# Optimization experiments

Hardware: AMD Instinct MI355X
Metric: run time of the kernel (lower is better)

## Reference

```python
import jax, jax.numpy as jnp
import numpy as np

DIM = 1152
NUM_HEADS = 16
HEAD_DIM = DIM // NUM_HEADS
EPS = 1e-6
B, N, M = 4, 4096, 512


def setup_inputs() -> dict:
    key = jax.random.key(0)
    ks = jax.random.split(key, 12)
    s = 0.02
    return {
        "x": jax.random.normal(ks[0], (B, N, DIM), dtype=jnp.float32),
        "cond": jax.random.normal(ks[1], (B, M, DIM), dtype=jnp.float32),
        "kv_seqlen": jax.random.randint(ks[2], (B,), 1, M + 1, dtype=jnp.int32),
        "q_w": jax.random.normal(ks[3], (DIM, DIM), dtype=jnp.float32) * s,
        "q_b": jnp.zeros((DIM,), jnp.float32),
        "kv_w": jax.random.normal(ks[4], (DIM, 2 * DIM), dtype=jnp.float32) * s,
        "kv_b": jnp.zeros((2 * DIM,), jnp.float32),
        "proj_w": jax.random.normal(ks[5], (DIM, DIM), dtype=jnp.float32) * s,
        "proj_b": jnp.zeros((DIM,), jnp.float32),
        "qn_w": jnp.ones((HEAD_DIM,), jnp.float32),
        "kn_w": jnp.ones((HEAD_DIM,), jnp.float32),
    }


def _rmsnorm_fp32(t, w):
    # RMSNorm computed in fp32 over head_dim, then cast back
    t32 = t.astype(jnp.float32)
    inv = jax.lax.rsqrt(jnp.mean(t32 * t32, axis=-1, keepdims=True) + EPS)
    return ((t32 * inv) * w.astype(jnp.float32)).astype(t.dtype)


def reference(x, cond, kv_seqlen, q_w, q_b, kv_w, kv_b, proj_w, proj_b, qn_w, kn_w):
    b, n, c = x.shape
    out_dtype = x.dtype
    q = (x @ q_w + q_b).reshape(b, n, NUM_HEADS, HEAD_DIM)           # [B,N,H,D]
    kv = (cond @ kv_w + kv_b).reshape(b, -1, 2, NUM_HEADS, HEAD_DIM)
    k, v = kv[:, :, 0], kv[:, :, 1]                                   # [B,M,H,D]
    q = _rmsnorm_fp32(q, qn_w)
    k = _rmsnorm_fp32(k, kn_w)
    # original casts to bf16 for the attention kernel when out_dtype is fp32
    q16, k16, v16 = q.astype(jnp.bfloat16), k.astype(jnp.bfloat16), v.astype(jnp.bfloat16)
    scale = 1.0 / np.sqrt(HEAD_DIM)
    scores = jnp.einsum("bnhd,bmhd->bhnm", q16, k16,
                        preferred_element_type=jnp.float32) * scale   # [B,H,N,M] fp32
    m = cond.shape[1]
    valid = (jnp.arange(m)[None, :] < kv_seqlen[:, None])             # [B,M] ragged kv mask
    scores = jnp.where(valid[:, None, None, :], scores, -jnp.inf)
    probs = jax.nn.softmax(scores, axis=-1).astype(jnp.bfloat16)
    out = jnp.einsum("bhnm,bmhd->bnhd", probs, v16).reshape(b, n, c)
    out = out.astype(out_dtype)
    return out @ proj_w + proj_b
```

## Files before the change

kernel.cpp:

```cpp
#include <hip/hip_runtime.h>
#include <math.h>

typedef unsigned short ushort_t;
typedef __attribute__((ext_vector_type(4))) float floatx4;
typedef __attribute__((ext_vector_type(8))) short bf16x8;

#define DIMC 1152
#define NHEADS 16
#define HDIM 72

__device__ __forceinline__ ushort_t f2bf(float f) {
  unsigned u = __float_as_uint(f);
  u += 0x7FFFu + ((u >> 16) & 1u);
  return (ushort_t)(u >> 16);
}
__device__ __forceinline__ float bf2f(ushort_t s) {
  return __uint_as_float(((unsigned)s) << 16);
}

__device__ __forceinline__ void gload_lds16(const ushort_t* g, ushort_t* l) {
  __builtin_amdgcn_global_load_lds(
      (const __attribute__((address_space(1))) unsigned int*)(const void*)g,
      (__attribute__((address_space(3))) unsigned int*)(void*)l, 16, 0, 0);
}

__device__ __forceinline__ bf16x8 load_bf16x8(const ushort_t* p) {
  union { bf16x8 v; uint4 u; } t;
  t.u = *(const uint4*)p;
  return t.v;
}

__global__ void cvt_bf16_kernel(const float* __restrict__ src,
                                ushort_t* __restrict__ dst, int n8) {
  int i = blockIdx.x * 256 + threadIdx.x;
  if (i >= n8) return;
  float4 f0 = ((const float4*)src)[2 * (size_t)i];
  float4 f1 = ((const float4*)src)[2 * (size_t)i + 1];
  union { ushort_t s[8]; uint4 u; } t;
  t.s[0] = f2bf(f0.x); t.s[1] = f2bf(f0.y); t.s[2] = f2bf(f0.z); t.s[3] = f2bf(f0.w);
  t.s[4] = f2bf(f1.x); t.s[5] = f2bf(f1.y); t.s[6] = f2bf(f1.z); t.s[7] = f2bf(f1.w);
  ((uint4*)dst)[i] = t.u;
}

__global__ void transpose_w_kernel(const float* __restrict__ W,
                                   ushort_t* __restrict__ Wt, int K, int N) {
  __shared__ ushort_t tile[64 * 80];
  int k0 = blockIdx.x * 64, n0 = blockIdx.y * 64;
  int tid = threadIdx.x;
  int kl = tid >> 4, n4 = tid & 15;
  for (int rr = 0; rr < 4; rr++) {
    int k = kl + rr * 16;
    float4 f = *(const float4*)(W + (size_t)(k0 + k) * N + n0 + n4 * 4);
    tile[(n4 * 4 + 0) * 80 + k] = f2bf(f.x);
    tile[(n4 * 4 + 1) * 80 + k] = f2bf(f.y);
    tile[(n4 * 4 + 2) * 80 + k] = f2bf(f.z);
    tile[(n4 * 4 + 3) * 80 + k] = f2bf(f.w);
  }
  __syncthreads();
  int nl = tid >> 2, kq = tid & 3;
  uint4 v0 = *(const uint4*)(tile + nl * 80 + kq * 16);
  uint4 v1 = *(const uint4*)(tile + nl * 80 + kq * 16 + 8);
  *(uint4*)(Wt + (size_t)(n0 + nl) * K + k0 + kq * 16) = v0;
  *(uint4*)(Wt + (size_t)(n0 + nl) * K + k0 + kq * 16 + 8) = v1;
}

template <bool OUT_F32>
__global__ __launch_bounds__(256, 3) void gemm128_kernel(
    const ushort_t* __restrict__ A0, const ushort_t* __restrict__ Bt0,
    const float* __restrict__ bias0, void* __restrict__ C0,
    int NTn0, int Ncols0,
    const ushort_t* __restrict__ A1, const ushort_t* __restrict__ Bt1,
    const float* __restrict__ bias1, void* __restrict__ C1,
    int NTn1, int Ncols1,
    int nblk0, int Kdim) {
  __shared__ ushort_t S[24576];

  int lin = blockIdx.x;
  int cpx = gridDim.x >> 3;
  int wg = (lin & 7) * cpx + (lin >> 3);

  const ushort_t* Aseg; const ushort_t* Bseg;
  const float* bias; void* Cptr; int NTn, Ncols;
  if (wg < nblk0) {
    Aseg = A0; Bseg = Bt0; bias = bias0; Cptr = C0; NTn = NTn0; Ncols = Ncols0;
  } else {
    wg -= nblk0;
    Aseg = A1; Bseg = Bt1; bias = bias1; Cptr = C1; NTn = NTn1; Ncols = Ncols1;
  }
  int mt = wg / NTn, nt = wg % NTn;
  int m0 = mt * 128, n0 = nt * 128;

  int tid = threadIdx.x;
  int wid = tid >> 6, lane = tid & 63, quad = lane >> 4, l16 = lane & 15;
  int wr = wid >> 1, wc = wid & 1;
  const int qoff = (quad * 8) ^ ((l16 & 8) << 1);

  const int srow = tid >> 2;
  const int scol = ((tid & 3) * 8) ^ ((tid & 32) ? 16 : 0);
  const ushort_t* Abase = Aseg + (size_t)m0 * Kdim;
  const ushort_t* Bbase = Bseg + (size_t)n0 * Kdim;

  auto stageA = [&](int t, int buf) {
    const ushort_t* src = Abase + (size_t)srow * Kdim + t * 32 + scol;
    ushort_t* dst = S + buf * 8192 + (tid >> 6) * 512;
    gload_lds16(src, dst);
    gload_lds16(src + (size_t)64 * Kdim, dst + 2048);
  };
  auto stageB = [&](int t, int buf) {
    const ushort_t* src = Bbase + (size_t)srow * Kdim + t * 32 + scol;
    ushort_t* dst = S + buf * 8192 + 4096 + (tid >> 6) * 512;
    gload_lds16(src, dst);
    gload_lds16(src + (size_t)64 * Kdim, dst + 2048);
  };

  floatx4 zero = {0.f, 0.f, 0.f, 0.f};
  floatx4 acc[4][4];
#pragma unroll
  for (int i = 0; i < 4; i++)
#pragma unroll
    for (int j = 0; j < 4; j++) acc[i][j] = zero;

  int NT = Kdim >> 5;

  stageA(0, 0); stageB(0, 0);
  stageA(1, 1); stageB(1, 1);
  asm volatile("s_waitcnt vmcnt(4)" ::: "memory");
  __builtin_amdgcn_s_barrier();

  int cur = 0;
  for (int t = 0; t < NT; ++t) {
    int nx2 = cur + 2; if (nx2 >= 3) nx2 -= 3;
    const int base = cur * 8192;
    const int arow = base + (wr * 64 + l16) * 32 + qoff;
    const int brow = base + 4096 + (wc * 64 + l16) * 32 + qoff;

    bf16x8 bfr[4], a01[2];
#pragma unroll
    for (int c = 0; c < 4; c++)
      bfr[c] = *(const bf16x8*)(S + brow + c * 512);
    a01[0] = *(const bf16x8*)(S + arow);
    a01[1] = *(const bf16x8*)(S + arow + 512);
    if (t + 2 < NT) stageA(t + 2, nx2);
    __builtin_amdgcn_s_barrier();
    asm volatile("s_waitcnt lgkmcnt(0)" ::: "memory");
    __builtin_amdgcn_sched_barrier(0);
    __builtin_amdgcn_s_setprio(1);
#pragma unroll
    for (int c = 0; c < 4; c++) {
      acc[0][c] = __builtin_amdgcn_mfma_f32_16x16x32_bf16(a01[0], bfr[c], acc[0][c], 0, 0, 0);
      acc[1][c] = __builtin_amdgcn_mfma_f32_16x16x32_bf16(a01[1], bfr[c], acc[1][c], 0, 0, 0);
    }
    __builtin_amdgcn_s_setprio(0);
    __builtin_amdgcn_s_barrier();

    bf16x8 a23[2];
    a23[0] = *(const bf16x8*)(S + arow + 1024);
    a23[1] = *(const bf16x8*)(S + arow + 1536);
    if (t + 2 < NT) stageB(t + 2, nx2);
    __builtin_amdgcn_s_barrier();
    asm volatile("s_waitcnt lgkmcnt(0)" ::: "memory");
    __builtin_amdgcn_sched_barrier(0);
    __builtin_amdgcn_s_setprio(1);
#pragma unroll
    for (int c = 0; c < 4; c++) {
      acc[2][c] = __builtin_amdgcn_mfma_f32_16x16x32_bf16(a23[0], bfr[c], acc[2][c], 0, 0, 0);
      acc[3][c] = __builtin_amdgcn_mfma_f32_16x16x32_bf16(a23[1], bfr[c], acc[3][c], 0, 0, 0);
    }
    __builtin_amdgcn_s_setprio(0);
    if (t + 2 < NT)
      asm volatile("s_waitcnt vmcnt(4)" ::: "memory");
    else
      asm volatile("s_waitcnt vmcnt(0)" ::: "memory");
    __builtin_amdgcn_s_barrier();

    cur = cur + 1; if (cur == 3) cur = 0;
  }

  float bv[4];
#pragma unroll
  for (int c = 0; c < 4; c++) bv[c] = bias[n0 + wc * 64 + c * 16 + l16];
#pragma unroll
  for (int mf = 0; mf < 4; mf++)
#pragma unroll
    for (int c = 0; c < 4; c++)
#pragma unroll
      for (int r = 0; r < 4; r++) {
        int row = m0 + wr * 64 + mf * 16 + quad * 4 + r;
        int col = n0 + wc * 64 + c * 16 + l16;
        float v = acc[mf][c][r] + bv[c];
        if constexpr (OUT_F32)
          ((float*)Cptr)[(size_t)row * Ncols + col] = v;
        else
          ((ushort_t*)Cptr)[(size_t)row * Ncols + col] = f2bf(v);
      }
}

__global__ void rmsnorm_heads_kernel(ushort_t* __restrict__ p,
                                     const float* __restrict__ w,
                                     int rowstride) {
  int gw = blockIdx.x * 4 + (threadIdx.x >> 6);
  int lane = threadIdx.x & 63;
  int row = gw >> 4, h = gw & 15;
  ushort_t* base = p + (size_t)row * rowstride + h * HDIM;
  float v0 = bf2f(base[lane]);
  float v1 = (lane < 8) ? bf2f(base[64 + lane]) : 0.f;
  float ss = v0 * v0 + v1 * v1;
  for (int off = 1; off < 64; off <<= 1) ss += __shfl_xor(ss, off);
  float inv = rsqrtf(ss / 72.0f + 1e-6f);
  base[lane] = f2bf(v0 * inv * w[lane]);
  if (lane < 8) base[64 + lane] = f2bf(v1 * inv * w[64 + lane]);
}

__global__ void vtrans_kernel(const ushort_t* __restrict__ kv16,
                              ushort_t* __restrict__ vT) {
  __shared__ ushort_t tile[64 * 84];
  int b = blockIdx.z, h = blockIdx.y, m0 = blockIdx.x * 64;
  int tid = threadIdx.x;
  int row = tid >> 2, sl = tid & 3;
  const ushort_t* src =
      kv16 + (size_t)(b * 512 + m0 + row) * 2304 + DIMC + h * HDIM;
#pragma unroll
  for (int k = 0; k < 5; k++) {
    int s = sl + 4 * k;
    if (s < 18) {
      uint2 v = *(const uint2*)(src + s * 4);
      *(uint2*)(tile + row * 84 + s * 4) = v;
    }
  }
  __syncthreads();
  size_t dbase = (size_t)((b * 16 + h) * 80) * 512 + m0;
#pragma unroll
  for (int it = 0; it < 5; it++) {
    int idx = it * 256 + tid;
    int d = idx >> 4, mseg = idx & 15;
    union { ushort_t s[4]; uint2 u; } pk;
    if (d < HDIM) {
      pk.s[0] = tile[(mseg * 4 + 0) * 84 + d];
      pk.s[1] = tile[(mseg * 4 + 1) * 84 + d];
      pk.s[2] = tile[(mseg * 4 + 2) * 84 + d];
      pk.s[3] = tile[(mseg * 4 + 3) * 84 + d];
    } else {
      ushort_t f = (d == HDIM) ? (ushort_t)0x3F80 : (ushort_t)0;
      pk.s[0] = pk.s[1] = pk.s[2] = pk.s[3] = f;
    }
    *(uint2*)(vT + dbase + (size_t)d * 512 + mseg * 4) = pk.u;
  }
}

__global__ __launch_bounds__(256, 4) void attn_kernel(
    const ushort_t* __restrict__ q16, const ushort_t* __restrict__ kv16,
    const ushort_t* __restrict__ vT, const int* __restrict__ seqlens,
    const float* __restrict__ qn_w, ushort_t* __restrict__ att) {
  __shared__ ushort_t KV[22 * 512];
  __shared__ ushort_t Ps[4][32 * 64];
  int b = blockIdx.z, h = blockIdx.y, n0 = blockIdx.x * 128;
  int tid = threadIdx.x, wid = tid >> 6, lane = tid & 63;
  int quad = lane >> 4, l16 = lane & 15;
  int seqlen = seqlens[b];
  const float qscale = 0.11785113019775793f * 1.44269504088896f;

  ushort_t* Pw = &Ps[wid][0];

  bf16x8 qf[2][3];
  float ssq[2] = {0.f, 0.f};
  for (int rb = 0; rb < 2; rb++)
    for (int ks = 0; ks < 3; ks++) {
      if (ks == 2 && quad > 0) {
        qf[rb][ks] = (bf16x8){0, 0, 0, 0, 0, 0, 0, 0};
      } else {
        size_t off = ((size_t)(b * 4096 + n0 + wid * 32 + rb * 16 + l16)) * DIMC +
                     h * HDIM + ks * 32 + quad * 8;
        qf[rb][ks] = load_bf16x8(q16 + off);
        union { bf16x8 v; ushort_t s[8]; } e;
        e.v = qf[rb][ks];
        for (int j = 0; j < 8; j++) {
          float x = bf2f(e.s[j]);
          ssq[rb] += x * x;
        }
      }
    }
  for (int rb = 0; rb < 2; rb++) {
    ssq[rb] += __shfl_xor(ssq[rb], 16);
    ssq[rb] += __shfl_xor(ssq[rb], 32);
  }
  for (int rb = 0; rb < 2; rb++) {
    float inv = rsqrtf(ssq[rb] / 72.0f + 1e-6f) * qscale;
    for (int ks = 0; ks < 3; ks++) {
      if (ks == 2 && quad > 0) continue;
      float4 w0 = *(const float4*)(qn_w + ks * 32 + quad * 8);
      float4 w1 = *(const float4*)(qn_w + ks * 32 + quad * 8 + 4);
      union { bf16x8 v; ushort_t s[8]; } e;
      e.v = qf[rb][ks];
      e.s[0] = f2bf(bf2f(e.s[0]) * inv * w0.x);
      e.s[1] = f2bf(bf2f(e.s[1]) * inv * w0.y);
      e.s[2] = f2bf(bf2f(e.s[2]) * inv * w0.z);
      e.s[3] = f2bf(bf2f(e.s[3]) * inv * w0.w);
      e.s[4] = f2bf(bf2f(e.s[4]) * inv * w1.x);
      e.s[5] = f2bf(bf2f(e.s[5]) * inv * w1.y);
      e.s[6] = f2bf(bf2f(e.s[6]) * inv * w1.z);
      e.s[7] = f2bf(bf2f(e.s[7]) * inv * w1.w);
      qf[rb][ks] = e.v;
    }
  }

  floatx4 zero = {0.f, 0.f, 0.f, 0.f};
  floatx4 of[2][5];
  for (int rb = 0; rb < 2; rb++)
    for (int nf = 0; nf < 5; nf++) of[rb][nf] = zero;

  const size_t kvrow = (size_t)b * 512;
  const size_t vbase = (size_t)((b * 16 + h) * 80) * 512;

  int ntiles = (seqlen + 63) >> 6;
  for (int mt = 0; mt < ntiles; mt++) {
    int m0 = mt * 64;

    __syncthreads();
    for (int id = wid; id < 22; id += 4) {
      const ushort_t* src;
      if (id < 12) {
        int c = (id * 11) >> 5;
        int ks = id - c * 3;
        src = kv16 + (size_t)(kvrow + m0 + c * 16 + l16) * 2304 + h * HDIM +
              ks * 32 + quad * 8;
      } else {
        int v = id - 12;
        int nf = v >> 1, ks = v & 1;
        src = vT + (vbase + (size_t)(nf * 16 + l16) * 512) + m0 + ks * 32 + quad * 8;
      }
      gload_lds16(src, KV + id * 512);
    }
    __syncthreads();

    floatx4 sf[2][4];
    for (int rb = 0; rb < 2; rb++)
      for (int c = 0; c < 4; c++) sf[rb][c] = zero;
    for (int c = 0; c < 4; c++)
      for (int ks = 0; ks < 3; ks++) {
        bf16x8 kf = *(const bf16x8*)(KV + (c * 3 + ks) * 512 + lane * 8);
        for (int rb = 0; rb < 2; rb++)
          sf[rb][c] = __builtin_amdgcn_mfma_f32_16x16x32_bf16(qf[rb][ks], kf, sf[rb][c], 0, 0, 0);
      }

    for (int rb = 0; rb < 2; rb++)
      for (int c = 0; c < 4; c++) {
        bool valid = (m0 + c * 16 + l16) < seqlen;
        int col = (c * 16 + l16) ^ (quad * 16);
        int rowb = rb * 16 + quad * 4;
        for (int r = 0; r < 4; r++) {
          float pp = valid ? __builtin_amdgcn_exp2f(sf[rb][c][r]) : 0.f;
          Pw[(rowb + r) * 64 + col] = f2bf(pp);
        }
      }

    for (int ks = 0; ks < 2; ks++) {
      bf16x8 pf[2];
      int g = ((ks * 2 + (quad >> 1)) * 16 + (quad & 1) * 8) ^ (((l16 >> 2) & 3) * 16);
      for (int rb = 0; rb < 2; rb++)
        pf[rb] = *(const bf16x8*)(Pw + (rb * 16 + l16) * 64 + g);
      for (int nf = 0; nf < 5; nf++) {
        bf16x8 vf = *(const bf16x8*)(KV + (12 + nf * 2 + ks) * 512 + lane * 8);
        for (int rb = 0; rb < 2; rb++)
          of[rb][nf] = __builtin_amdgcn_mfma_f32_16x16x32_bf16(pf[rb], vf, of[rb][nf], 0, 0, 0);
      }
    }
  }

  for (int rb = 0; rb < 2; rb++) {
    float invl[4];
    for (int r = 0; r < 4; r++) {
      float lsum = __shfl(of[rb][4][r], (lane & 48) | 8);
      invl[r] = 1.0f / lsum;
    }
    for (int nf = 0; nf < 5; nf++) {
      int d = nf * 16 + l16;
      if (d < HDIM) {
        for (int r = 0; r < 4; r++) {
          size_t o = ((size_t)(b * 4096 + n0 + wid * 32 + rb * 16 + quad * 4 + r)) * DIMC +
                     h * HDIM + d;
          att[o] = f2bf(of[rb][nf][r] * invl[r]);
        }
      }
    }
  }
}

extern "C" void kernel_launch(void* const* d_in, const int* in_sizes, int n_in,
                              void* d_out, int out_size, void* d_ws, size_t ws_size,
                              hipStream_t stream) {
  const float* x      = (const float*)d_in[0];
  const float* cond   = (const float*)d_in[1];
  const int*   seqlen = (const int*)d_in[2];
  const float* q_w    = (const float*)d_in[3];
  const float* q_b    = (const float*)d_in[4];
  const float* kv_w   = (const float*)d_in[5];
  const float* kv_b   = (const float*)d_in[6];
  const float* proj_w = (const float*)d_in[7];
  const float* proj_b = (const float*)d_in[8];
  const float* qn_w   = (const float*)d_in[9];
  const float* kn_w   = (const float*)d_in[10];
  float* out = (float*)d_out;

  char* ws = (char*)d_ws;
  size_t o = 0;
  ushort_t* qwT    = (ushort_t*)(ws + o); o += (size_t)1152 * 1152 * 2;
  ushort_t* kvwT   = (ushort_t*)(ws + o); o += (size_t)2304 * 1152 * 2;
  ushort_t* pwT    = (ushort_t*)(ws + o); o += (size_t)1152 * 1152 * 2;
  ushort_t* q16    = (ushort_t*)(ws + o); o += (size_t)16384 * 1152 * 2;
  ushort_t* kv16   = (ushort_t*)(ws + o); o += (size_t)2048 * 2304 * 2;
  ushort_t* vT     = (ushort_t*)(ws + o); o += (size_t)64 * 80 * 512 * 2;
  ushort_t* att    = (ushort_t*)(ws + o); o += (size_t)16384 * 1152 * 2;
  ushort_t* x16    = (ushort_t*)(ws + o); o += (size_t)16384 * 1152 * 2;
  ushort_t* cond16 = (ushort_t*)(ws + o); o += (size_t)2048 * 1152 * 2;

  dim3 blk(256);

  cvt_bf16_kernel<<<dim3((16384 * 1152 / 8 + 255) / 256), blk, 0, stream>>>(
      x, x16, 16384 * 1152 / 8);
  cvt_bf16_kernel<<<dim3((2048 * 1152 / 8 + 255) / 256), blk, 0, stream>>>(
      cond, cond16, 2048 * 1152 / 8);

  transpose_w_kernel<<<dim3(1152 / 64, 1152 / 64), blk, 0, stream>>>(q_w, qwT, 1152, 1152);
  transpose_w_kernel<<<dim3(1152 / 64, 2304 / 64), blk, 0, stream>>>(kv_w, kvwT, 1152, 2304);
  transpose_w_kernel<<<dim3(1152 / 64, 1152 / 64), blk, 0, stream>>>(proj_w, pwT, 1152, 1152);

  gemm128_kernel<false><<<dim3(1152 + 288), blk, 0, stream>>>(
      x16, qwT, q_b, q16, 9, 1152,
      cond16, kvwT, kv_b, kv16, 18, 2304,
      1152, 1152);

  rmsnorm_heads_kernel<<<dim3(2048 * 16 / 4), blk, 0, stream>>>(kv16, kn_w, 2304);

  vtrans_kernel<<<dim3(8, 16, 4), blk, 0, stream>>>(kv16, vT);

  attn_kernel<<<dim3(32, 16, 4), blk, 0, stream>>>(q16, kv16, vT, seqlen, qn_w, att);

  gemm128_kernel<true><<<dim3(1152), blk, 0, stream>>>(
      att, pwT, proj_b, out, 9, 1152,
      att, pwT, proj_b, out, 9, 1152,
      1152, 1152);
}
```

Baseline: 375.8 us.

## Switch GEMM to double-buffered BK=64 stages with per-k-slice prefetch

The GEMM main loop moves from a triple-buffered 32-wide K pipeline to a double-buffered 64-wide K tile split into two 32-wide sub-steps. Each sub-step loads all A and B fragments, prefetches the matching slice of the next tile, and issues 16 MFMAs. This halves the barrier count per K element and gives larger MFMA batches between syncs. LDS grows to 64 KB per block and launch bounds drop to 2 blocks per CU, so occupancy falls.

```diff
diff --git a/kernel.cpp b/kernel.cpp
--- a/kernel.cpp
+++ b/kernel.cpp
@@ -65,7 +65,7 @@
 }
 
 template <bool OUT_F32>
-__global__ __launch_bounds__(256, 3) void gemm128_kernel(
+__global__ __launch_bounds__(256, 2) void gemm128_kernel(
     const ushort_t* __restrict__ A0, const ushort_t* __restrict__ Bt0,
     const float* __restrict__ bias0, void* __restrict__ C0,
     int NTn0, int Ncols0,
@@ -73,7 +73,7 @@
     const float* __restrict__ bias1, void* __restrict__ C1,
     int NTn1, int Ncols1,
     int nblk0, int Kdim) {
-  __shared__ ushort_t S[24576];
+  __shared__ ushort_t S[32768];
 
   int lin = blockIdx.x;
   int cpx = gridDim.x >> 3;
@@ -100,15 +100,15 @@
   const ushort_t* Abase = Aseg + (size_t)m0 * Kdim;
   const ushort_t* Bbase = Bseg + (size_t)n0 * Kdim;
 
-  auto stageA = [&](int t, int buf) {
-    const ushort_t* src = Abase + (size_t)srow * Kdim + t * 32 + scol;
-    ushort_t* dst = S + buf * 8192 + (tid >> 6) * 512;
+  auto stageA = [&](int t, int ks) {
+    const ushort_t* src = Abase + (size_t)srow * Kdim + t * 64 + ks * 32 + scol;
+    ushort_t* dst = S + (t & 1) * 16384 + ks * 4096 + (tid >> 6) * 512;
     gload_lds16(src, dst);
     gload_lds16(src + (size_t)64 * Kdim, dst + 2048);
   };
-  auto stageB = [&](int t, int buf) {
-    const ushort_t* src = Bbase + (size_t)srow * Kdim + t * 32 + scol;
-    ushort_t* dst = S + buf * 8192 + 4096 + (tid >> 6) * 512;
+  auto stageB = [&](int t, int ks) {
+    const ushort_t* src = Bbase + (size_t)srow * Kdim + t * 64 + ks * 32 + scol;
+    ushort_t* dst = S + (t & 1) * 16384 + 8192 + ks * 4096 + (tid >> 6) * 512;
     gload_lds16(src, dst);
     gload_lds16(src + (size_t)64 * Kdim, dst + 2048);
   };
@@ -120,60 +120,46 @@
 #pragma unroll
     for (int j = 0; j < 4; j++) acc[i][j] = zero;
 
-  int NT = Kdim >> 5;
+  int NT = Kdim >> 6;
 
   stageA(0, 0); stageB(0, 0);
-  stageA(1, 1); stageB(1, 1);
+  stageA(0, 1); stageB(0, 1);
   asm volatile("s_waitcnt vmcnt(4)" ::: "memory");
   __builtin_amdgcn_s_barrier();
 
-  int cur = 0;
   for (int t = 0; t < NT; ++t) {
-    int nx2 = cur + 2; if (nx2 >= 3) nx2 -= 3;
-    const int base = cur * 8192;
-    const int arow = base + (wr * 64 + l16) * 32 + qoff;
-    const int brow = base + 4096 + (wc * 64 + l16) * 32 + qoff;
-
-    bf16x8 bfr[4], a01[2];
-#pragma unroll
-    for (int c = 0; c < 4; c++)
-      bfr[c] = *(const bf16x8*)(S + brow + c * 512);
-    a01[0] = *(const bf16x8*)(S + arow);
-    a01[1] = *(const bf16x8*)(S + arow + 512);
-    if (t + 2 < NT) stageA(t + 2, nx2);
-    __builtin_amdgcn_s_barrier();
-    asm volatile("s_waitcnt lgkmcnt(0)" ::: "memory");
-    __builtin_amdgcn_sched_barrier(0);
-    __builtin_amdgcn_s_setprio(1);
-#pragma unroll
-    for (int c = 0; c < 4; c++) {
-      acc[0][c] = __builtin_amdgcn_mfma_f32_16x16x32_bf16(a01[0], bfr[c], acc[0][c], 0, 0, 0);
-      acc[1][c] = __builtin_amdgcn_mfma_f32_16x16x32_bf16(a01[1], bfr[c], acc[1][c], 0, 0, 0);
-    }
-    __builtin_amdgcn_s_setprio(0);
-    __builtin_amdgcn_s_barrier();
-
-    bf16x8 a23[2];
-    a23[0] = *(const bf16x8*)(S + arow + 1024);
-    a23[1] = *(const bf16x8*)(S + arow + 1536);
-    if (t + 2 < NT) stageB(t + 2, nx2);
-    __builtin_amdgcn_s_barrier();
-    asm volatile("s_waitcnt lgkmcnt(0)" ::: "memory");
-    __builtin_amdgcn_sched_barrier(0);
-    __builtin_amdgcn_s_setprio(1);
-#pragma unroll
-    for (int c = 0; c < 4; c++) {
-      acc[2][c] = __builtin_amdgcn_mfma_f32_16x16x32_bf16(a23[0], bfr[c], acc[2][c], 0, 0, 0);
-      acc[3][c] = __builtin_amdgcn_mfma_f32_16x16x32_bf16(a23[1], bfr[c], acc[3][c], 0, 0, 0);
-    }
-    __builtin_amdgcn_s_setprio(0);
-    if (t + 2 < NT)
-      asm volatile("s_waitcnt vmcnt(4)" ::: "memory");
-    else
-      asm volatile("s_waitcnt vmcnt(0)" ::: "memory");
-    __builtin_amdgcn_s_barrier();
-
-    cur = cur + 1; if (cur == 3) cur = 0;
+    const int abase = (t & 1) * 16384;
+    const int arow = (wr * 64 + l16) * 32 + qoff;
+    const int brow = (wc * 64 + l16) * 32 + qoff;
+
+#pragma unroll
+    for (int ks = 0; ks < 2; ++ks) {
+      const int ab = abase + ks * 4096;
+      const int bb = abase + 8192 + ks * 4096;
+      bf16x8 af[4], bfr[4];
+#pragma unroll
+      for (int mf = 0; mf < 4; mf++)
+        af[mf] = *(const bf16x8*)(S + ab + arow + mf * 512);
+#pragma unroll
+      for (int c = 0; c < 4; c++)
+        bfr[c] = *(const bf16x8*)(S + bb + brow + c * 512);
+      if (t + 1 < NT) { stageA(t + 1, ks); stageB(t + 1, ks); }
+      __builtin_amdgcn_s_barrier();
+      asm volatile("s_waitcnt lgkmcnt(0)" ::: "memory");
+      __builtin_amdgcn_sched_barrier(0);
+      __builtin_amdgcn_s_setprio(1);
+#pragma unroll
+      for (int c = 0; c < 4; c++)
+#pragma unroll
+        for (int mf = 0; mf < 4; mf++)
+          acc[mf][c] = __builtin_amdgcn_mfma_f32_16x16x32_bf16(af[mf], bfr[c], acc[mf][c], 0, 0, 0);
+      __builtin_amdgcn_s_setprio(0);
+      if (t + 1 < NT)
+        asm volatile("s_waitcnt vmcnt(4)" ::: "memory");
+      else
+        asm volatile("s_waitcnt vmcnt(0)" ::: "memory");
+      __builtin_amdgcn_s_barrier();
+    }
   }
 
   float bv[4];
```

Result: no change. 380.9 us (+1.4%).
